# Optimization experiments

Hardware: AMD Instinct MI355X
Metric: run time of the kernel (lower is better)

The kernel has to match this reference:

```python
import jax, jax.numpy as jnp
import numpy as np

B, T, C, H = 128, 256, 1024, 64


def setup_inputs() -> dict:
    key = jax.random.key(0)
    k1, k2, k3, k4 = jax.random.split(key, 4)
    # Glorot-ish scale for weights
    s = 1.0 / np.sqrt(C)
    return {
        "x": jax.random.normal(k1, (B, T, C), dtype=jnp.float32),
        "Wk": jax.random.normal(k2, (C, H), dtype=jnp.float32) * s,
        "Wq": jax.random.normal(k3, (C, H), dtype=jnp.float32) * s,
        "Wv": jax.random.normal(k4, (C, H), dtype=jnp.float32) * s,
    }


def reference(x, Wk, Wq, Wv):
    # Projections (no bias, matching use_bias=False)
    k = jnp.einsum("btc,ch->bth", x, Wk)  # [B,T,H]
    q = jnp.einsum("btc,ch->bth", x, Wq)
    v = jnp.einsum("btc,ch->bth", x, Wv)
    scale = k.shape[-1] ** -0.5
    wei = jnp.einsum("bth,bsh->bts", q, k) * scale  # [B,T,T]
    t = x.shape[1]
    causal = jnp.tril(jnp.ones((t, t), dtype=bool))
    wei = jnp.where(causal, wei, -jnp.inf)
    wei = jax.nn.softmax(wei, axis=-1)
    # dropout is identity at inference
    out = jnp.einsum("bts,bsh->bth", wei, v)  # [B,T,H]
    return out
```

## Files before the change

### kernel.cpp

```cpp
#include <hip/hip_runtime.h>
#include <hip/hip_bf16.h>

typedef __bf16 v8bf __attribute__((ext_vector_type(8)));
typedef float f32x16 __attribute__((ext_vector_type(16)));
typedef unsigned int uint;
typedef unsigned short ushort;

#define GLOAD16(gsrc, ldst)                                                       \
  __builtin_amdgcn_global_load_lds(                                               \
      (const __attribute__((address_space(1))) unsigned int*)(gsrc),              \
      (__attribute__((address_space(3))) unsigned int*)(ldst), 16, 0, 0)

__device__ inline f32x16 zero16() {
  f32x16 z;
#pragma unroll
  for (int i = 0; i < 16; i++) z[i] = 0.f;
  return z;
}

__device__ inline uint pack_bf16(float a, float b) {
  union { __bf16 h[2]; uint u; } c;
  c.h[0] = (__bf16)a;
  c.h[1] = (__bf16)b;
  return c.u;
}

__global__ void prep_wt(const float* __restrict__ Wq, const float* __restrict__ Wk,
                        const float* __restrict__ Wv, char* __restrict__ Wt_s) {
  __shared__ __bf16 tile[64][74];
  const int mat = blockIdx.x >> 4;
  const int c0 = (blockIdx.x & 15) * 64;
  const float* src = (mat == 0) ? Wq : (mat == 1) ? Wk : Wv;
  const int t = threadIdx.x;
  {
    const int r = t >> 2;
    const int ch = (t & 3) * 16;
    const float4* s4 = (const float4*)(src + (size_t)(c0 + r) * 64 + ch);
#pragma unroll
    for (int j = 0; j < 4; j++) {
      float4 f = s4[j];
      tile[r][ch + 4 * j + 0] = (__bf16)f.x;
      tile[r][ch + 4 * j + 1] = (__bf16)f.y;
      tile[r][ch + 4 * j + 2] = (__bf16)f.z;
      tile[r][ch + 4 * j + 3] = (__bf16)f.w;
    }
  }
  __syncthreads();
  const int h = t >> 2;
  const int cc = (t & 3) * 16;
  union { __bf16 o[16]; uint4 u[2]; } pk;
#pragma unroll
  for (int j = 0; j < 16; j++) pk.o[j] = tile[cc + j][h];
  const int n = mat * 64 + h;
  char* base = Wt_s + (size_t)n * 2048 + (c0 >> 6) * 128;
  const int bc = cc * 2;
  *(uint4*)(base + ((bc) ^ ((n & 7) << 4))) = pk.u[0];
  *(uint4*)(base + ((bc + 16) ^ ((n & 7) << 4))) = pk.u[1];
}

__launch_bounds__(256, 2)
__global__ void proj_kernel(const float* __restrict__ x, const char* __restrict__ Wt_s,
                            __bf16* __restrict__ Qa, char* __restrict__ Ka,
                            __bf16* __restrict__ Va) {
  __shared__ char lds[65536];
  char* A0 = lds;
  char* A1 = lds + 8192;
  char* W0 = lds + 16384;
  char* W1 = lds + 40960;

  const int tid = threadIdx.x;
  const int lane = tid & 63;
  const int wave = tid >> 6;
  const int wm = wave >> 1;
  const int wn = wave & 1;
  const int row0 = blockIdx.x * 64;

  const int sr = tid >> 2;
  const int sc = tid & 3;
  const float4* xp = (const float4*)(x + (size_t)(row0 + sr) * 1024 + sc * 16);

  f32x16 acc[3];
#pragma unroll
  for (int i = 0; i < 3; i++) acc[i] = zero16();

  float4 s0[4], s1[4], s2[4], s3[4];

#define SB __builtin_amdgcn_sched_barrier(0)

#define LOADA(rr, t)                                                              \
  {                                                                               \
    _Pragma("unroll") for (int j = 0; j < 4; j++) rr[j] = xp[(t) * 16 + j];       \
  }

#define GW(t, Wbuf)                                                               \
  {                                                                               \
    _Pragma("unroll") for (int j = 0; j < 6; j++) {                               \
      int idx = wave * 64 + j * 256 + lane;                                       \
      GLOAD16(Wt_s + (size_t)(idx >> 3) * 2048 + (t) * 128 + (idx & 7) * 16,      \
              Wbuf + wave * 1024 + j * 4096);                                     \
    }                                                                             \
  }

#define CVTWRITE(rr, Abuf)                                                        \
  {                                                                               \
    union { __bf16 h[16]; uint4 u[2]; } cv;                                       \
    _Pragma("unroll") for (int j = 0; j < 4; j++) {                               \
      cv.h[4 * j + 0] = (__bf16)rr[j].x;                                          \
      cv.h[4 * j + 1] = (__bf16)rr[j].y;                                          \
      cv.h[4 * j + 2] = (__bf16)rr[j].z;                                          \
      cv.h[4 * j + 3] = (__bf16)rr[j].w;                                          \
    }                                                                             \
    *(uint4*)(Abuf + sr * 128 + ((sc * 32) ^ ((sr & 7) << 4))) = cv.u[0];         \
    *(uint4*)(Abuf + sr * 128 + ((sc * 32 + 16) ^ ((sr & 7) << 4))) = cv.u[1];    \
  }

#define MMA(Abuf, Wbuf)                                                           \
  {                                                                               \
    _Pragma("unroll") for (int ks = 0; ks < 4; ks++) {                            \
      int arow = wm * 32 + (lane & 31);                                           \
      int kb = ks * 32 + ((lane >> 5) << 4);                                      \
      v8bf av = *(const v8bf*)(Abuf + arow * 128 + (kb ^ ((arow & 7) << 4)));     \
      _Pragma("unroll") for (int nf = 0; nf < 3; nf++) {                          \
        int brow = wn * 96 + nf * 32 + (lane & 31);                               \
        v8bf bv = *(const v8bf*)(Wbuf + brow * 128 + (kb ^ ((brow & 7) << 4)));   \
        acc[nf] = __builtin_amdgcn_mfma_f32_32x32x16_bf16(av, bv, acc[nf], 0, 0, 0); \
      }                                                                           \
    }                                                                             \
  }

#define BAR4                                                                      \
  do {                                                                            \
    asm volatile("s_waitcnt vmcnt(4) lgkmcnt(0)" ::: "memory");                   \
    __builtin_amdgcn_s_barrier();                                                 \
    SB;                                                                           \
  } while (0)
#define BAR0                                                                      \
  do {                                                                            \
    asm volatile("s_waitcnt vmcnt(0) lgkmcnt(0)" ::: "memory");                   \
    __builtin_amdgcn_s_barrier();                                                 \
    SB;                                                                           \
  } while (0)

#define STEP(T, SI, SC_, ACUR, WCUR, ANXT, WNXT)                                  \
  GW(T + 1, WNXT);                                                                \
  SB;                                                                             \
  LOADA(SI, T + 2);                                                               \
  SB;                                                                             \
  MMA(ACUR, WCUR);                                                                \
  CVTWRITE(SC_, ANXT);                                                            \
  BAR4;

  GW(0, W0);
  SB;
  LOADA(s0, 0);
  LOADA(s1, 1);
  SB;
  CVTWRITE(s0, A0);
  BAR4;

  STEP(0, s2, s1, A0, W0, A1, W1)
  STEP(1, s3, s2, A1, W1, A0, W0)
  STEP(2, s0, s3, A0, W0, A1, W1)
  STEP(3, s1, s0, A1, W1, A0, W0)
  STEP(4, s2, s1, A0, W0, A1, W1)
  STEP(5, s3, s2, A1, W1, A0, W0)
  STEP(6, s0, s3, A0, W0, A1, W1)
  STEP(7, s1, s0, A1, W1, A0, W0)
  STEP(8, s2, s1, A0, W0, A1, W1)
  STEP(9, s3, s2, A1, W1, A0, W0)
  STEP(10, s0, s3, A0, W0, A1, W1)
  STEP(11, s1, s0, A1, W1, A0, W0)
  STEP(12, s2, s1, A0, W0, A1, W1)
  STEP(13, s3, s2, A1, W1, A0, W0)
  GW(15, W1);
  SB;
  MMA(A0, W0);
  CVTWRITE(s3, A1);
  BAR0;
  MMA(A1, W1);

#pragma unroll
  for (int nf = 0; nf < 3; nf++) {
    const int colb = wn * 96 + nf * 32;
#pragma unroll
    for (int r = 0; r < 16; r++) {
      int g = row0 + wm * 32 + (r & 3) + ((r >> 2) << 3) + ((lane >> 5) << 2);
      __bf16 val = (__bf16)acc[nf][r];
      if (colb < 64) {
        Qa[(size_t)g * 64 + colb + (lane & 31)] = val;
      } else if (colb < 128) {
        int h = colb - 64 + (lane & 31);
        int s = g & 255, bb = g >> 8;
        int byte = s * 128 + ((h * 2) ^ ((s & 7) << 4));
        *(__bf16*)(Ka + (size_t)bb * 32768 + byte) = val;
      } else {
        Va[(size_t)g * 64 + colb - 128 + (lane & 31)] = val;
      }
    }
  }
#undef STEP
#undef BAR4
#undef BAR0
#undef LOADA
#undef GW
#undef CVTWRITE
#undef MMA
#undef SB
}

__launch_bounds__(256)
__global__ void attn_kernel(const __bf16* __restrict__ Qa, const char* __restrict__ Ka,
                            const __bf16* __restrict__ Va, float* __restrict__ out) {
  __shared__ char lds[65536];
  char* Klds = lds;
  char* Vlds = lds + 32768;

  const int tid = threadIdx.x;
  const int lane = tid & 63;
  const int wave = tid >> 6;
  const int b = blockIdx.x >> 1;
  const int half = blockIdx.x & 1;
  const int bt0 = half * 128;

  v8bf bq[4];
  {
    const __bf16* qsrc = Qa + (size_t)(b * 256 + bt0 + wave * 32 + (lane & 31)) * 64 +
                         ((lane >> 5) << 3);
#pragma unroll
    for (int ks = 0; ks < 4; ks++) bq[ks] = *(const v8bf*)(qsrc + ks * 16);
  }

  {
    const char* ksrc = Ka + (size_t)b * 32768 + wave * 1024 + lane * 16;
#pragma unroll
    for (int i = 0; i < 8; i++)
      GLOAD16(ksrc + i * 4096, Klds + wave * 1024 + i * 4096);
  }
  {
    int s = tid;
    const uint4* src = (const uint4*)(Va + (size_t)(b * 256 + s) * 64);
#pragma unroll
    for (int i = 0; i < 8; i++) {
      uint4 v = src[i];
      const ushort* e = (const ushort*)&v;
#pragma unroll
      for (int j = 0; j < 8; j++) {
        int h = i * 8 + j;
        int byte = h * 512 + ((s * 2) ^ ((h & 7) << 4));
        *(ushort*)(Vlds + byte) = e[j];
      }
    }
  }
  __syncthreads();

  const int t0 = bt0 + wave * 32;
  const int tg = t0 + (lane & 31);
  const int nf = (t0 >> 5) + 1;

  f32x16 sacc[8];
#pragma unroll
  for (int sf = 0; sf < 8; sf++) {
    f32x16 sv = zero16();
    if (sf < nf) {
#pragma unroll
      for (int ks = 0; ks < 4; ks++) {
        int kbyte = ks * 32 + ((lane >> 5) << 4);
        int krow = sf * 32 + (lane & 31);
        v8bf a = *(const v8bf*)(Klds + krow * 128 + (kbyte ^ ((krow & 7) << 4)));
        sv = __builtin_amdgcn_mfma_f32_32x32x16_bf16(a, bq[ks], sv, 0, 0, 0);
      }
    }
    sacc[sf] = sv;
  }

  float m = -1e30f;
#pragma unroll
  for (int sf = 0; sf < 8; sf++) {
    if (sf < nf) {
#pragma unroll
      for (int r = 0; r < 16; r++) {
        int sg = sf * 32 + (r & 3) + ((r >> 2) << 3) + ((lane >> 5) << 2);
        float v = sacc[sf][r] * 0.125f;
        v = (sg > tg) ? -1e30f : v;
        sacc[sf][r] = v;
        m = fmaxf(m, v);
      }
    }
  }
  m = fmaxf(m, __shfl_xor(m, 32, 64));
  float l = 0.f;
#pragma unroll
  for (int sf = 0; sf < 8; sf++) {
    if (sf < nf) {
#pragma unroll
      for (int r = 0; r < 16; r++) {
        float p = __expf(sacc[sf][r] - m);
        sacc[sf][r] = p;
        l += p;
      }
    }
  }
  l += __shfl_xor(l, 32, 64);
  float inv = 1.0f / l;

  f32x16 oacc[2];
  oacc[0] = zero16();
  oacc[1] = zero16();
  const bool hiLane = (lane >= 32);
#pragma unroll
  for (int sf = 0; sf < 8; sf++) {
    if (sf < nf) {
      uint w[8], ow[8];
#pragma unroll
      for (int q = 0; q < 4; q++) {
        w[2 * q]     = pack_bf16(sacc[sf][4 * q] * inv,     sacc[sf][4 * q + 1] * inv);
        w[2 * q + 1] = pack_bf16(sacc[sf][4 * q + 2] * inv, sacc[sf][4 * q + 3] * inv);
      }
#pragma unroll
      for (int i = 0; i < 8; i++) ow[i] = (uint)__shfl_xor((int)w[i], 32, 64);
#pragma unroll
      for (int ks = 0; ks < 2; ks++) {
        int bse = 4 * ks;
        union { uint u[4]; v8bf v; } A;
        A.u[0] = hiLane ? ow[bse + 2] : w[bse + 0];
        A.u[1] = hiLane ? ow[bse + 3] : w[bse + 1];
        A.u[2] = hiLane ? w[bse + 2] : ow[bse + 0];
        A.u[3] = hiLane ? w[bse + 3] : ow[bse + 1];
        int sbyte0 = (sf * 32 + ks * 16) * 2 + ((lane >> 5) << 4);
#pragma unroll
        for (int hf = 0; hf < 2; hf++) {
          int vrow = hf * 32 + (lane & 31);
          v8bf bv = *(const v8bf*)(Vlds + vrow * 512 + (sbyte0 ^ ((vrow & 7) << 4)));
          oacc[hf] = __builtin_amdgcn_mfma_f32_32x32x16_bf16(A.v, bv, oacc[hf], 0, 0, 0);
        }
      }
    }
  }

#pragma unroll
  for (int hf = 0; hf < 2; hf++) {
#pragma unroll
    for (int r = 0; r < 16; r++) {
      int t = t0 + (r & 3) + ((r >> 2) << 3) + ((lane >> 5) << 2);
      int h = hf * 32 + (lane & 31);
      out[((size_t)b * 256 + t) * 64 + h] = oacc[hf][r];
    }
  }
}

extern "C" void kernel_launch(void* const* d_in, const int* in_sizes, int n_in,
                              void* d_out, int out_size, void* d_ws, size_t ws_size,
                              hipStream_t stream) {
  const float* x  = (const float*)d_in[0];
  const float* Wk = (const float*)d_in[1];
  const float* Wq = (const float*)d_in[2];
  const float* Wv = (const float*)d_in[3];
  float* out = (float*)d_out;

  __bf16* Qa = (__bf16*)d_ws;
  char* Ka   = (char*)d_ws + 4194304;
  __bf16* Va = (__bf16*)((char*)d_ws + 8388608);
  char* Wt_s = (char*)d_ws + 12582912;

  prep_wt<<<48, 256, 0, stream>>>(Wq, Wk, Wv, Wt_s);
  proj_kernel<<<512, 256, 0, stream>>>(x, Wt_s, Qa, Ka, Va);
  attn_kernel<<<256, 256, 0, stream>>>(Qa, Ka, Va, out);
}
```

Before: 47.75 us.

## Fuse QKV projection and causal attention into one per-batch kernel

Merges the projection and attention kernels into a single kernel with one 512-thread block per batch. Q, K and V are written straight into LDS instead of round-tripping through global workspace. This removes a kernel launch and the global writes and reads of the intermediates. In exchange the grid shrinks from 512 plus 256 blocks to 128 blocks on a GPU with many more CUs, and LDS use grows to 112KB per block, which limits occupancy.

```diff
diff --git a/kernel.cpp b/kernel.cpp
--- a/kernel.cpp
+++ b/kernel.cpp
@@ -58,97 +58,101 @@
   *(uint4*)(base + ((bc + 16) ^ ((n & 7) << 4))) = pk.u[1];
 }
 
-__launch_bounds__(256, 2)
-__global__ void proj_kernel(const float* __restrict__ x, const char* __restrict__ Wt_s,
-                            __bf16* __restrict__ Qa, char* __restrict__ Ka,
-                            __bf16* __restrict__ Va) {
-  __shared__ char lds[65536];
+__launch_bounds__(512, 2)
+__global__ void fused_kernel(const float* __restrict__ x, const char* __restrict__ Wt_s,
+                             float* __restrict__ out) {
+  __shared__ char lds[114688];
   char* A0 = lds;
-  char* A1 = lds + 8192;
-  char* W0 = lds + 16384;
-  char* W1 = lds + 40960;
+  char* A1 = lds + 32768;
+  char* W0 = lds + 65536;
+  char* W1 = lds + 90112;
+  char* Qlds = lds;
+  char* Klds = lds + 32768;
+  char* Vlds = lds + 65536;
 
   const int tid = threadIdx.x;
   const int lane = tid & 63;
   const int wave = tid >> 6;
-  const int wm = wave >> 1;
-  const int wn = wave & 1;
-  const int row0 = blockIdx.x * 64;
-
-  const int sr = tid >> 2;
-  const int sc = tid & 3;
-  const float4* xp = (const float4*)(x + (size_t)(row0 + sr) * 1024 + sc * 16);
-
-  f32x16 acc[3];
-#pragma unroll
-  for (int i = 0; i < 3; i++) acc[i] = zero16();
-
-  float4 s0[4], s1[4], s2[4], s3[4];
+  const int b = blockIdx.x;
+  const int row0 = b * 256;
+  const int hi = lane >> 5;
+
+  const int sr = tid >> 1;
+  const int sc = tid & 1;
+  const float4* xp = (const float4*)(x + (size_t)(row0 + sr) * 1024) + sc * 8;
+
+  f32x16 acc[6];
+#pragma unroll
+  for (int i = 0; i < 6; i++) acc[i] = zero16();
+
+  float4 s0[8], s1[8];
 
 #define SB __builtin_amdgcn_sched_barrier(0)
 
-#define LOADA(rr, t)                                                              \
+#define LOADA(rr, T)                                                              \
   {                                                                               \
-    _Pragma("unroll") for (int j = 0; j < 4; j++) rr[j] = xp[(t) * 16 + j];       \
-  }
-
-#define GW(t, Wbuf)                                                               \
+    _Pragma("unroll") for (int j = 0; j < 8; j++) rr[j] = xp[(T) * 16 + j];       \
+  }
+
+#define GW(T, Wbuf)                                                               \
   {                                                                               \
-    _Pragma("unroll") for (int j = 0; j < 6; j++) {                               \
-      int idx = wave * 64 + j * 256 + lane;                                       \
-      GLOAD16(Wt_s + (size_t)(idx >> 3) * 2048 + (t) * 128 + (idx & 7) * 16,      \
-              Wbuf + wave * 1024 + j * 4096);                                     \
+    _Pragma("unroll") for (int j = 0; j < 3; j++) {                               \
+      int idx = j * 512 + tid;                                                    \
+      GLOAD16(Wt_s + (size_t)(idx >> 3) * 2048 + (T) * 128 + (idx & 7) * 16,      \
+              Wbuf + j * 8192 + wave * 1024);                                     \
     }                                                                             \
   }
 
 #define CVTWRITE(rr, Abuf)                                                        \
   {                                                                               \
-    union { __bf16 h[16]; uint4 u[2]; } cv;                                       \
-    _Pragma("unroll") for (int j = 0; j < 4; j++) {                               \
+    union { __bf16 h[32]; uint4 u[4]; } cv;                                       \
+    _Pragma("unroll") for (int j = 0; j < 8; j++) {                               \
       cv.h[4 * j + 0] = (__bf16)rr[j].x;                                          \
       cv.h[4 * j + 1] = (__bf16)rr[j].y;                                          \
       cv.h[4 * j + 2] = (__bf16)rr[j].z;                                          \
       cv.h[4 * j + 3] = (__bf16)rr[j].w;                                          \
     }                                                                             \
-    *(uint4*)(Abuf + sr * 128 + ((sc * 32) ^ ((sr & 7) << 4))) = cv.u[0];         \
-    *(uint4*)(Abuf + sr * 128 + ((sc * 32 + 16) ^ ((sr & 7) << 4))) = cv.u[1];    \
+    _Pragma("unroll") for (int j = 0; j < 4; j++) {                               \
+      *(uint4*)(Abuf + sr * 128 + (((sc * 64) + j * 16) ^ ((sr & 7) << 4))) =     \
+          cv.u[j];                                                                \
+    }                                                                             \
   }
 
 #define MMA(Abuf, Wbuf)                                                           \
   {                                                                               \
     _Pragma("unroll") for (int ks = 0; ks < 4; ks++) {                            \
-      int arow = wm * 32 + (lane & 31);                                           \
-      int kb = ks * 32 + ((lane >> 5) << 4);                                      \
+      int arow = wave * 32 + (lane & 31);                                         \
+      int kb = ks * 32 + (hi << 4);                                               \
       v8bf av = *(const v8bf*)(Abuf + arow * 128 + (kb ^ ((arow & 7) << 4)));     \
-      _Pragma("unroll") for (int nf = 0; nf < 3; nf++) {                          \
-        int brow = wn * 96 + nf * 32 + (lane & 31);                               \
+      _Pragma("unroll") for (int nf = 0; nf < 6; nf++) {                          \
+        int brow = nf * 32 + (lane & 31);                                         \
         v8bf bv = *(const v8bf*)(Wbuf + brow * 128 + (kb ^ ((brow & 7) << 4)));   \
         acc[nf] = __builtin_amdgcn_mfma_f32_32x32x16_bf16(av, bv, acc[nf], 0, 0, 0); \
       }                                                                           \
     }                                                                             \
   }
 
-#define BAR4                                                                      \
+#define BAR8                                                                      \
   do {                                                                            \
-    asm volatile("s_waitcnt vmcnt(4) lgkmcnt(0)" ::: "memory");                   \
+    asm volatile("s_waitcnt vmcnt(8) lgkmcnt(0)" ::: "memory");                   \
     __builtin_amdgcn_s_barrier();                                                 \
     SB;                                                                           \
   } while (0)
-#define BAR0                                                                      \
+#define BAR0v                                                                     \
   do {                                                                            \
     asm volatile("s_waitcnt vmcnt(0) lgkmcnt(0)" ::: "memory");                   \
     __builtin_amdgcn_s_barrier();                                                 \
     SB;                                                                           \
   } while (0)
 
-#define STEP(T, SI, SC_, ACUR, WCUR, ANXT, WNXT)                                  \
+#define STEP(T, SCUR, SNXT, ACUR, WCUR, ANXT, WNXT)                               \
   GW(T + 1, WNXT);                                                                \
   SB;                                                                             \
-  LOADA(SI, T + 2);                                                               \
+  LOADA(SCUR, (T) + 2);                                                           \
   SB;                                                                             \
   MMA(ACUR, WCUR);                                                                \
-  CVTWRITE(SC_, ANXT);                                                            \
-  BAR4;
+  CVTWRITE(SNXT, ANXT);                                                           \
+  BAR8;
 
   GW(0, W0);
   SB;
@@ -156,115 +160,72 @@
   LOADA(s1, 1);
   SB;
   CVTWRITE(s0, A0);
-  BAR4;
-
-  STEP(0, s2, s1, A0, W0, A1, W1)
-  STEP(1, s3, s2, A1, W1, A0, W0)
-  STEP(2, s0, s3, A0, W0, A1, W1)
+  BAR8;
+
+  STEP(0, s0, s1, A0, W0, A1, W1)
+  STEP(1, s1, s0, A1, W1, A0, W0)
+  STEP(2, s0, s1, A0, W0, A1, W1)
   STEP(3, s1, s0, A1, W1, A0, W0)
-  STEP(4, s2, s1, A0, W0, A1, W1)
-  STEP(5, s3, s2, A1, W1, A0, W0)
-  STEP(6, s0, s3, A0, W0, A1, W1)
+  STEP(4, s0, s1, A0, W0, A1, W1)
+  STEP(5, s1, s0, A1, W1, A0, W0)
+  STEP(6, s0, s1, A0, W0, A1, W1)
   STEP(7, s1, s0, A1, W1, A0, W0)
-  STEP(8, s2, s1, A0, W0, A1, W1)
-  STEP(9, s3, s2, A1, W1, A0, W0)
-  STEP(10, s0, s3, A0, W0, A1, W1)
+  STEP(8, s0, s1, A0, W0, A1, W1)
+  STEP(9, s1, s0, A1, W1, A0, W0)
+  STEP(10, s0, s1, A0, W0, A1, W1)
   STEP(11, s1, s0, A1, W1, A0, W0)
-  STEP(12, s2, s1, A0, W0, A1, W1)
-  STEP(13, s3, s2, A1, W1, A0, W0)
+  STEP(12, s0, s1, A0, W0, A1, W1)
+  STEP(13, s1, s0, A1, W1, A0, W0)
   GW(15, W1);
   SB;
   MMA(A0, W0);
-  CVTWRITE(s3, A1);
-  BAR0;
+  CVTWRITE(s1, A1);
+  BAR0v;
   MMA(A1, W1);
 
-#pragma unroll
-  for (int nf = 0; nf < 3; nf++) {
-    const int colb = wn * 96 + nf * 32;
+  __syncthreads();
+#pragma unroll
+  for (int nf = 0; nf < 6; nf++) {
 #pragma unroll
     for (int r = 0; r < 16; r++) {
-      int g = row0 + wm * 32 + (r & 3) + ((r >> 2) << 3) + ((lane >> 5) << 2);
+      int g = wave * 32 + (r & 3) + ((r >> 2) << 3) + (hi << 2);
+      int col = nf * 32 + (lane & 31);
       __bf16 val = (__bf16)acc[nf][r];
-      if (colb < 64) {
-        Qa[(size_t)g * 64 + colb + (lane & 31)] = val;
-      } else if (colb < 128) {
-        int h = colb - 64 + (lane & 31);
-        int s = g & 255, bb = g >> 8;
-        int byte = s * 128 + ((h * 2) ^ ((s & 7) << 4));
-        *(__bf16*)(Ka + (size_t)bb * 32768 + byte) = val;
+      if (nf < 2) {
+        *(__bf16*)(Qlds + g * 128 + ((col * 2) ^ ((g & 7) << 4))) = val;
+      } else if (nf < 4) {
+        int h = col - 64;
+        *(__bf16*)(Klds + g * 128 + ((h * 2) ^ ((g & 7) << 4))) = val;
       } else {
-        Va[(size_t)g * 64 + colb - 128 + (lane & 31)] = val;
-      }
-    }
-  }
-#undef STEP
-#undef BAR4
-#undef BAR0
-#undef LOADA
-#undef GW
-#undef CVTWRITE
-#undef MMA
-#undef SB
-}
-
-__launch_bounds__(256)
-__global__ void attn_kernel(const __bf16* __restrict__ Qa, const char* __restrict__ Ka,
-                            const __bf16* __restrict__ Va, float* __restrict__ out) {
-  __shared__ char lds[65536];
-  char* Klds = lds;
-  char* Vlds = lds + 32768;
-
-  const int tid = threadIdx.x;
-  const int lane = tid & 63;
-  const int wave = tid >> 6;
-  const int b = blockIdx.x >> 1;
-  const int half = blockIdx.x & 1;
-  const int bt0 = half * 128;
+        int h = col - 128;
+        *(__bf16*)(Vlds + h * 512 + ((g * 2) ^ ((h & 7) << 4))) = val;
+      }
+    }
+  }
+  __syncthreads();
+
+  const int t0 = wave * 32;
+  const int tg = t0 + (lane & 31);
+  const int nfr = wave + 1;
 
   v8bf bq[4];
   {
-    const __bf16* qsrc = Qa + (size_t)(b * 256 + bt0 + wave * 32 + (lane & 31)) * 64 +
-                         ((lane >> 5) << 3);
-#pragma unroll
-    for (int ks = 0; ks < 4; ks++) bq[ks] = *(const v8bf*)(qsrc + ks * 16);
-  }
-
-  {
-    const char* ksrc = Ka + (size_t)b * 32768 + wave * 1024 + lane * 16;
-#pragma unroll
-    for (int i = 0; i < 8; i++)
-      GLOAD16(ksrc + i * 4096, Klds + wave * 1024 + i * 4096);
-  }
-  {
-    int s = tid;
-    const uint4* src = (const uint4*)(Va + (size_t)(b * 256 + s) * 64);
-#pragma unroll
-    for (int i = 0; i < 8; i++) {
-      uint4 v = src[i];
-      const ushort* e = (const ushort*)&v;
-#pragma unroll
-      for (int j = 0; j < 8; j++) {
-        int h = i * 8 + j;
-        int byte = h * 512 + ((s * 2) ^ ((h & 7) << 4));
-        *(ushort*)(Vlds + byte) = e[j];
-      }
-    }
-  }
-  __syncthreads();
-
-  const int t0 = bt0 + wave * 32;
-  const int tg = t0 + (lane & 31);
-  const int nf = (t0 >> 5) + 1;
+    int qrow = wave * 32 + (lane & 31);
+#pragma unroll
+    for (int ks = 0; ks < 4; ks++) {
+      int kbyte = ks * 32 + (hi << 4);
+      bq[ks] = *(const v8bf*)(Qlds + qrow * 128 + (kbyte ^ ((qrow & 7) << 4)));
+    }
+  }
 
   f32x16 sacc[8];
 #pragma unroll
   for (int sf = 0; sf < 8; sf++) {
     f32x16 sv = zero16();
-    if (sf < nf) {
+    if (sf < nfr) {
 #pragma unroll
       for (int ks = 0; ks < 4; ks++) {
-        int kbyte = ks * 32 + ((lane >> 5) << 4);
+        int kbyte = ks * 32 + (hi << 4);
         int krow = sf * 32 + (lane & 31);
         v8bf a = *(const v8bf*)(Klds + krow * 128 + (kbyte ^ ((krow & 7) << 4)));
         sv = __builtin_amdgcn_mfma_f32_32x32x16_bf16(a, bq[ks], sv, 0, 0, 0);
@@ -276,10 +237,10 @@
   float m = -1e30f;
 #pragma unroll
   for (int sf = 0; sf < 8; sf++) {
-    if (sf < nf) {
+    if (sf < nfr) {
 #pragma unroll
       for (int r = 0; r < 16; r++) {
-        int sg = sf * 32 + (r & 3) + ((r >> 2) << 3) + ((lane >> 5) << 2);
+        int sg = sf * 32 + (r & 3) + ((r >> 2) << 3) + (hi << 2);
         float v = sacc[sf][r] * 0.125f;
         v = (sg > tg) ? -1e30f : v;
         sacc[sf][r] = v;
@@ -291,7 +252,7 @@
   float l = 0.f;
 #pragma unroll
   for (int sf = 0; sf < 8; sf++) {
-    if (sf < nf) {
+    if (sf < nfr) {
 #pragma unroll
       for (int r = 0; r < 16; r++) {
         float p = __expf(sacc[sf][r] - m);
@@ -309,7 +270,7 @@
   const bool hiLane = (lane >= 32);
 #pragma unroll
   for (int sf = 0; sf < 8; sf++) {
-    if (sf < nf) {
+    if (sf < nfr) {
       uint w[8], ow[8];
 #pragma unroll
       for (int q = 0; q < 4; q++) {
@@ -326,7 +287,7 @@
         A.u[1] = hiLane ? ow[bse + 3] : w[bse + 1];
         A.u[2] = hiLane ? w[bse + 2] : ow[bse + 0];
         A.u[3] = hiLane ? w[bse + 3] : ow[bse + 1];
-        int sbyte0 = (sf * 32 + ks * 16) * 2 + ((lane >> 5) << 4);
+        int sbyte0 = (sf * 32 + ks * 16) * 2 + (hi << 4);
 #pragma unroll
         for (int hf = 0; hf < 2; hf++) {
           int vrow = hf * 32 + (lane & 31);
@@ -341,11 +302,19 @@
   for (int hf = 0; hf < 2; hf++) {
 #pragma unroll
     for (int r = 0; r < 16; r++) {
-      int t = t0 + (r & 3) + ((r >> 2) << 3) + ((lane >> 5) << 2);
+      int t = t0 + (r & 3) + ((r >> 2) << 3) + (hi << 2);
       int h = hf * 32 + (lane & 31);
       out[((size_t)b * 256 + t) * 64 + h] = oacc[hf][r];
     }
   }
+#undef STEP
+#undef BAR8
+#undef BAR0v
+#undef LOADA
+#undef GW
+#undef CVTWRITE
+#undef MMA
+#undef SB
 }
 
 extern "C" void kernel_launch(void* const* d_in, const int* in_sizes, int n_in,
@@ -357,12 +326,8 @@
   const float* Wv = (const float*)d_in[3];
   float* out = (float*)d_out;
 
-  __bf16* Qa = (__bf16*)d_ws;
-  char* Ka   = (char*)d_ws + 4194304;
-  __bf16* Va = (__bf16*)((char*)d_ws + 8388608);
-  char* Wt_s = (char*)d_ws + 12582912;
+  char* Wt_s = (char*)d_ws;
 
   prep_wt<<<48, 256, 0, stream>>>(Wq, Wk, Wv, Wt_s);
-  proj_kernel<<<512, 256, 0, stream>>>(x, Wt_s, Qa, Ka, Va);
-  attn_kernel<<<256, 256, 0, stream>>>(Qa, Ka, Va, out);
-}
+  fused_kernel<<<128, 512, 0, stream>>>(x, Wt_s, out);
+}
```

Result: slower. 62.15 us (+30.1%).
